# Kernel tuning notes

Hardware: AMD Instinct MI355X
Metric: run time of the kernel (lower is better)

Reference implementation:

```python
import jax, jax.numpy as jnp
import numpy as np

N_NODES = 100000
N_EDGES = 3200000
N_GRAPHS = 64
IN_DIM = 128
EDGE_DIM = 16
HIDDEN = 64
LATENT = 16


def setup_inputs() -> dict:
    key = jax.random.key(0)
    ks = jax.random.split(key, 12)
    x = jax.random.normal(ks[0], (N_NODES, IN_DIM), dtype=jnp.float32)
    edge_feat = jax.random.normal(ks[1], (N_EDGES, EDGE_DIM), dtype=jnp.float32)
    src = jax.random.randint(ks[2], (N_EDGES,), 0, N_NODES)
    dst = jax.random.randint(ks[3], (N_EDGES,), 0, N_NODES)
    node_graph = jnp.sort(jax.random.randint(ks[4], (N_NODES,), 0, N_GRAPHS))
    s = lambda d: 1.0 / np.sqrt(d)
    W1 = jax.random.normal(ks[5], (IN_DIM, HIDDEN), dtype=jnp.float32) * s(IN_DIM)
    b1 = jnp.zeros((HIDDEN,), jnp.float32)
    W2 = jax.random.normal(ks[6], (HIDDEN, HIDDEN), dtype=jnp.float32) * s(HIDDEN)
    b2 = jnp.zeros((HIDDEN,), jnp.float32)
    We = jax.random.normal(ks[7], (EDGE_DIM, HIDDEN), dtype=jnp.float32) * s(EDGE_DIM)
    be = jnp.zeros((HIDDEN,), jnp.float32)
    Wmu = jax.random.normal(ks[8], (HIDDEN, LATENT), dtype=jnp.float32) * s(HIDDEN)
    bmu = jnp.zeros((LATENT,), jnp.float32)
    Wlv = jax.random.normal(ks[9], (HIDDEN, LATENT), dtype=jnp.float32) * s(HIDDEN)
    blv = jnp.zeros((LATENT,), jnp.float32)
    return {"x": x, "edge_feat": edge_feat, "src": src, "dst": dst,
            "node_graph": node_graph, "W1": W1, "b1": b1, "W2": W2, "b2": b2,
            "We": We, "be": be, "Wmu": Wmu, "bmu": bmu, "Wlv": Wlv, "blv": blv}


def _graph_conv(h, src, dst, W, b):
    # DGL GraphConv with norm='both', allow_zero_in_degree=True, ReLU activation.
    ones = jnp.ones((src.shape[0],), h.dtype)
    deg_out = jnp.clip(jax.ops.segment_sum(ones, src, num_segments=N_NODES), 1.0)
    deg_in = jnp.clip(jax.ops.segment_sum(ones, dst, num_segments=N_NODES), 1.0)
    # project first (cheaper when out <= in), then symmetric-normalized SpMM
    hw = h @ W  # [N, out]
    hw = hw * (deg_out ** -0.5)[:, None]
    agg = jax.ops.segment_sum(hw[src], dst, num_segments=N_NODES)
    agg = agg * (deg_in ** -0.5)[:, None]
    return jax.nn.relu(agg + b)


def reference(x, edge_feat, src, dst, node_graph, W1, b1, W2, b2, We, be,
              Wmu, bmu, Wlv, blv):
    h = _graph_conv(x, src, dst, W1, b1)
    h = _graph_conv(h, src, dst, W2, b2)
    # edge_fc is computed and stored in edata in the original, but does not
    # affect the (mu, logvar) outputs
    edge_h = edge_feat @ We + be  # noqa: F841 (kept for fidelity)
    # dgl.mean_nodes: per-graph mean of node features
    sums = jax.ops.segment_sum(h, node_graph, num_segments=N_GRAPHS)
    counts = jnp.clip(jax.ops.segment_sum(jnp.ones((N_NODES,), h.dtype),
                                          node_graph, num_segments=N_GRAPHS), 1.0)
    h_graph = sums / counts[:, None]  # [G, HIDDEN]
    mu = h_graph @ Wmu + bmu
    logvar = h_graph @ Wlv + blv
    return (mu, logvar)
```

## Files before the change

kernel.cpp:

```cpp
#include <hip/hip_runtime.h>
#include <hip/hip_fp16.h>

#define N_NODES 100000
#define N_EDGES 3200000
#define N_GRAPHS 64
#define IN_DIM 128
#define HIDDEN 64
#define LATENT 16

#define NB 1024
#define BSH 7
#define NB_USED 782
#define SC_BLOCKS 256
#define NKEYS 1024
#define NBLK_AGG 1563
#define SEG_INTS (1565 * 64)

__global__ __launch_bounds__(256) void zero_k(int4* __restrict__ p, int n4) {
  int i = blockIdx.x * 256 + threadIdx.x;
  if (i < n4) p[i] = make_int4(0, 0, 0, 0);
}

__global__ __launch_bounds__(256) void hist_c_k(const int4* __restrict__ src4,
                                                const int4* __restrict__ dst4,
                                                int* __restrict__ bc_src,
                                                int* __restrict__ bc_dst,
                                                int* __restrict__ tbl_src,
                                                int* __restrict__ tbl_dst) {
  __shared__ int hs[NB], hd[NB];
  int t = threadIdx.x;
  for (int i = t; i < NB; i += 256) { hs[i] = 0; hd[i] = 0; }
  __syncthreads();
  const int Q = N_EDGES / 4;
  const int QPB = Q / SC_BLOCKS;
  int q0 = blockIdx.x * QPB, q1 = q0 + QPB;
  for (int i = q0 + t; i < q1; i += 256) {
    int4 s = src4[i], d = dst4[i];
    atomicAdd(&hs[s.x >> BSH], 1); atomicAdd(&hs[s.y >> BSH], 1);
    atomicAdd(&hs[s.z >> BSH], 1); atomicAdd(&hs[s.w >> BSH], 1);
    atomicAdd(&hd[d.x >> BSH], 1); atomicAdd(&hd[d.y >> BSH], 1);
    atomicAdd(&hd[d.z >> BSH], 1); atomicAdd(&hd[d.w >> BSH], 1);
  }
  __syncthreads();
  for (int i = t; i < NB; i += 256) {
    int a = hs[i], b = hd[i];
    tbl_src[blockIdx.x * NB + i] = a;
    tbl_dst[blockIdx.x * NB + i] = b;
    if (a) atomicAdd(&bc_src[i], a);
    if (b) atomicAdd(&bc_dst[i], b);
  }
}

__global__ __launch_bounds__(256) void scan_c_k(const int* __restrict__ bc_src,
                                                const int* __restrict__ bc_dst,
                                                int* __restrict__ bbase_src,
                                                int* __restrict__ bbase_dst) {
  __shared__ int ts[256];
  int t = threadIdx.x;
  int b4 = 4 * t;
  {
    int a0 = bc_src[b4], a1 = bc_src[b4 + 1], a2 = bc_src[b4 + 2], a3 = bc_src[b4 + 3];
    int s = a0 + a1 + a2 + a3;
    ts[t] = s;
    __syncthreads();
    for (int off = 1; off < 256; off <<= 1) {
      int x = 0;
      if (t >= off) x = ts[t - off];
      __syncthreads();
      if (t >= off) ts[t] += x;
      __syncthreads();
    }
    int run = ts[t] - s;
    bbase_src[b4] = run;
    bbase_src[b4 + 1] = run + a0;
    bbase_src[b4 + 2] = run + a0 + a1;
    bbase_src[b4 + 3] = run + a0 + a1 + a2;
    if (t == 255) bbase_src[NB] = ts[255];
    __syncthreads();
  }
  {
    int a0 = bc_dst[b4], a1 = bc_dst[b4 + 1], a2 = bc_dst[b4 + 2], a3 = bc_dst[b4 + 3];
    int s = a0 + a1 + a2 + a3;
    ts[t] = s;
    __syncthreads();
    for (int off = 1; off < 256; off <<= 1) {
      int x = 0;
      if (t >= off) x = ts[t - off];
      __syncthreads();
      if (t >= off) ts[t] += x;
      __syncthreads();
    }
    int run = ts[t] - s;
    bbase_dst[b4] = run;
    bbase_dst[b4 + 1] = run + a0;
    bbase_dst[b4 + 2] = run + a0 + a1;
    bbase_dst[b4 + 3] = run + a0 + a1 + a2;
    if (t == 255) bbase_dst[NB] = ts[255];
  }
}

__global__ __launch_bounds__(256) void scatter_c_k(const int4* __restrict__ src4,
                                                   const int4* __restrict__ dst4,
                                                   const int* __restrict__ bbase_src,
                                                   const int* __restrict__ bbase_dst,
                                                   const int* __restrict__ tbl_src,
                                                   const int* __restrict__ tbl_dst,
                                                   int* __restrict__ cur_src,
                                                   int* __restrict__ cur_dst,
                                                   int* __restrict__ sortedS,
                                                   int* __restrict__ sortedE) {
  __shared__ int rs[NB], rd[NB];
  int t = threadIdx.x;
  for (int i = t; i < NB; i += 256) {
    int a = tbl_src[blockIdx.x * NB + i];
    int b = tbl_dst[blockIdx.x * NB + i];
    rs[i] = a ? (atomicAdd(&cur_src[i], a) + bbase_src[i]) : 0;
    rd[i] = b ? (atomicAdd(&cur_dst[i], b) + bbase_dst[i]) : 0;
  }
  __syncthreads();
  const int Q = N_EDGES / 4;
  const int QPB = Q / SC_BLOCKS;
  int q0 = blockIdx.x * QPB, q1 = q0 + QPB;
  for (int i = q0 + t; i < q1; i += 256) {
    int4 s = src4[i], d = dst4[i];
    int sv[4] = {s.x, s.y, s.z, s.w};
    int dv[4] = {d.x, d.y, d.z, d.w};
#pragma unroll
    for (int k = 0; k < 4; k++) {
      int ps = atomicAdd(&rs[sv[k] >> BSH], 1);
      sortedS[ps] = sv[k];
      int pd = atomicAdd(&rd[dv[k] >> BSH], 1);
      sortedE[pd] = ((dv[k] & 127) << 17) | sv[k];
    }
  }
}

__global__ __launch_bounds__(256) void fine_sort_k(const int* __restrict__ sortedE,
                                                   const int* __restrict__ bbase_dst,
                                                   int* __restrict__ deg_in,
                                                   int* __restrict__ seg,
                                                   int* __restrict__ eblk) {
  __shared__ int hist[NKEYS];
  __shared__ int cur[NKEYS];
  __shared__ int ts[256];
  int bk = blockIdx.x, t = threadIdx.x;
  int node0 = bk << BSH;
  int e0 = bbase_dst[bk], e1 = bbase_dst[bk + 1];
  for (int i = t; i < NKEYS; i += 256) hist[i] = 0;
  __syncthreads();
  for (int j = e0 + t; j < e1; j += 256) {
    int v = sortedE[j];
    int d7 = v >> 17, sr = v & 0x1FFFF;
    int key = ((d7 >> 6) << 9) | ((sr >> 14) << 6) | ((d7 & 7) << 3) | ((d7 >> 3) & 7);
    atomicAdd(&hist[key], 1);
  }
  __syncthreads();
  int b4 = 4 * t;
  int a0 = hist[b4], a1 = hist[b4 + 1], a2 = hist[b4 + 2], a3 = hist[b4 + 3];
  int s = a0 + a1 + a2 + a3;
  ts[t] = s;
  __syncthreads();
  for (int off = 1; off < 256; off <<= 1) {
    int x = 0;
    if (t >= off) x = ts[t - off];
    __syncthreads();
    if (t >= off) ts[t] += x;
    __syncthreads();
  }
  int run = ts[t] - s;
  cur[b4] = run;
  cur[b4 + 1] = run + a0;
  cur[b4 + 2] = run + a0 + a1;
  cur[b4 + 3] = run + a0 + a1 + a2;
  __syncthreads();
  if (t < 128) {
    int n = node0 + t;
    if (n < N_NODES) {
      int sub = t >> 6, o = t & 7, row = (t >> 3) & 7;
      int base = (sub << 9) | (o << 3) | row;
      int dg = 0;
#pragma unroll
      for (int c = 0; c < 8; c++) dg += hist[base + (c << 6)];
      deg_in[n] = dg;
    }
  }
  if (t < 128) {
    int sub = t >> 6, c = (t >> 3) & 7, o = t & 7;
    seg[(bk * 2 + sub) * 64 + c * 8 + o] = e0 + cur[(sub << 9) | (c << 6) | (o << 3)];
  }
  __syncthreads();
  for (int j = e0 + t; j < e1; j += 256) {
    int v = sortedE[j];
    int d7 = v >> 17, sr = v & 0x1FFFF;
    int key = ((d7 >> 6) << 9) | ((sr >> 14) << 6) | ((d7 & 7) << 3) | ((d7 >> 3) & 7);
    int pos = e0 + atomicAdd(&cur[key], 1);
    eblk[pos] = ((d7 & 63) << 17) | sr;
  }
}

__global__ __launch_bounds__(256) void degout_c_k(const int* __restrict__ sortedS,
                                                  const int* __restrict__ bbase_src,
                                                  int* __restrict__ deg_out) {
  __shared__ int h[128];
  int bk = blockIdx.x, t = threadIdx.x;
  if (t < 128) h[t] = 0;
  __syncthreads();
  int s0 = bbase_src[bk], s1 = bbase_src[bk + 1];
  for (int j = s0 + t; j < s1; j += 256) atomicAdd(&h[sortedS[j] & 127], 1);
  __syncthreads();
  if (t < 128) {
    int n = (bk << BSH) | t;
    if (n < N_NODES) deg_out[n] = h[t];
  }
}

__global__ __launch_bounds__(256) void counts_k(const int* __restrict__ node_graph,
                                                float* __restrict__ counts) {
  __shared__ int h[N_GRAPHS];
  int t = threadIdx.x;
  if (t < N_GRAPHS) h[t] = 0;
  __syncthreads();
  int base = blockIdx.x * 1024;
  int end = base + 1024; if (end > N_NODES) end = N_NODES;
  for (int i = base + t; i < end; i += 256) atomicAdd(&h[node_graph[i]], 1);
  __syncthreads();
  if (t < N_GRAPHS && h[t]) atomicAdd(&counts[t], (float)h[t]);
}

template <int IN, typename IT, typename OT>
__global__ __launch_bounds__(256) void gemm_tile_k(const IT* __restrict__ X,
                                                   const float* __restrict__ W,
                                                   const int* __restrict__ deg,
                                                   OT* __restrict__ out) {
  __shared__ float xs[64][IN + 4];
  __shared__ float ws[IN][HIDDEN];
  int t = threadIdx.x;
  int row0_blk = blockIdx.x * 64;

  for (int i = t; i < IN * HIDDEN / 4; i += 256)
    ((float4*)ws)[i] = ((const float4*)W)[i];
  for (int i = t; i < 64 * (IN / 4); i += 256) {
    int r = i / (IN / 4), c4 = i % (IN / 4);
    int row = row0_blk + r;
    float4 v = make_float4(0.f, 0.f, 0.f, 0.f);
    if (row < N_NODES) {
      if constexpr (sizeof(IT) == 4) {
        v = *(const float4*)&X[(size_t)row * IN + c4 * 4];
      } else {
        union { short4 s; __half2 h2[2]; } u;
        u.s = *(const short4*)&X[(size_t)row * IN + c4 * 4];
        float2 f0 = __half22float2(u.h2[0]);
        float2 f1 = __half22float2(u.h2[1]);
        v = make_float4(f0.x, f0.y, f1.x, f1.y);
      }
    }
    *(float4*)&xs[r][c4 * 4] = v;
  }
  __syncthreads();

  int w = t >> 6, lane = t & 63;
  int rg = lane >> 4, cg = lane & 15;
  int r0 = w * 16 + rg * 4;
  int c0 = cg * 4;

  float acc[4][4];
#pragma unroll
  for (int i = 0; i < 4; i++)
#pragma unroll
    for (int j = 0; j < 4; j++) acc[i][j] = 0.f;

#pragma unroll 4
  for (int d4 = 0; d4 < IN / 4; d4++) {
    float4 a0 = *(const float4*)&xs[r0 + 0][d4 * 4];
    float4 a1 = *(const float4*)&xs[r0 + 1][d4 * 4];
    float4 a2 = *(const float4*)&xs[r0 + 2][d4 * 4];
    float4 a3 = *(const float4*)&xs[r0 + 3][d4 * 4];
#pragma unroll
    for (int dd = 0; dd < 4; dd++) {
      float4 b = *(const float4*)&ws[d4 * 4 + dd][c0];
      float av0 = (&a0.x)[dd], av1 = (&a1.x)[dd], av2 = (&a2.x)[dd], av3 = (&a3.x)[dd];
      acc[0][0] += av0 * b.x; acc[0][1] += av0 * b.y; acc[0][2] += av0 * b.z; acc[0][3] += av0 * b.w;
      acc[1][0] += av1 * b.x; acc[1][1] += av1 * b.y; acc[1][2] += av1 * b.z; acc[1][3] += av1 * b.w;
      acc[2][0] += av2 * b.x; acc[2][1] += av2 * b.y; acc[2][2] += av2 * b.z; acc[2][3] += av2 * b.w;
      acc[3][0] += av3 * b.x; acc[3][1] += av3 * b.y; acc[3][2] += av3 * b.z; acc[3][3] += av3 * b.w;
    }
  }

#pragma unroll
  for (int i = 0; i < 4; i++) {
    int row = row0_blk + r0 + i;
    if (row >= N_NODES) continue;
    float dg = (float)deg[row];
    if (dg < 1.f) dg = 1.f;
    float sc = rsqrtf(dg);
    if constexpr (sizeof(OT) == 2) {
      __half2 p0 = __floats2half2_rn(acc[i][0] * sc, acc[i][1] * sc);
      __half2 p1 = __floats2half2_rn(acc[i][2] * sc, acc[i][3] * sc);
      union { __half2 h2[2]; float2 f2; } u;
      u.h2[0] = p0; u.h2[1] = p1;
      *(float2*)&out[(size_t)row * HIDDEN + c0] = u.f2;
    } else {
      float4 o = make_float4(acc[i][0] * sc, acc[i][1] * sc, acc[i][2] * sc, acc[i][3] * sc);
      *(float4*)&out[(size_t)row * HIDDEN + c0] = o;
    }
  }
}

template <int MODE>
__global__ __launch_bounds__(256) void agg_seg_k(const __half* __restrict__ A,
                                                 const int* __restrict__ eblk,
                                                 const int* __restrict__ seg,
                                                 const int* __restrict__ deg_in,
                                                 const float* __restrict__ bias,
                                                 const float* __restrict__ W2,
                                                 const int* __restrict__ deg_out,
                                                 const int* __restrict__ node_graph,
                                                 float* __restrict__ sums,
                                                 __half* __restrict__ out) {
  __shared__ float acc[64][68];
  __shared__ int ngs[64];
  __shared__ float psum[4][64];
  int bk = blockIdx.x, t = threadIdx.x;
  int o = t >> 5, l = t & 31;
  for (int i = t; i < 64 * 68; i += 256) ((float*)acc)[i] = 0.f;
  __syncthreads();
  int segbase = bk * 64;
  float rx = 0.f, ry = 0.f;
  int cur_d = -1;
#pragma unroll
  for (int c = 0; c < 8; c++) {
    int j0 = seg[segbase + c * 8 + o];
    int j1 = seg[segbase + c * 8 + o + 1];
    int j = j0;
    for (; j + 16 <= j1; j += 16) {
      int ev = eblk[j + (l & 15)];
      int vv[16];
#pragma unroll
      for (int k = 0; k < 16; k++) vv[k] = __shfl(ev, k, 32);
      float2 ff[16];
#pragma unroll
      for (int k = 0; k < 16; k++)
        ff[k] = __half22float2(*(const __half2*)&A[(size_t)(vv[k] & 0x1FFFF) * HIDDEN + 2 * l]);
#pragma unroll
      for (int k = 0; k < 16; k++) {
        int d = vv[k] >> 17;
        if (d != cur_d) {
          if (cur_d >= 0) {
            float2* ap = (float2*)&acc[cur_d][2 * l];
            float2 a0 = *ap; a0.x += rx; a0.y += ry; *ap = a0;
          }
          cur_d = d; rx = 0.f; ry = 0.f;
        }
        rx += ff[k].x; ry += ff[k].y;
      }
    }
    for (; j + 4 <= j1; j += 4) {
      int vv[4];
#pragma unroll
      for (int k = 0; k < 4; k++) vv[k] = eblk[j + k];
      float2 ff[4];
#pragma unroll
      for (int k = 0; k < 4; k++)
        ff[k] = __half22float2(*(const __half2*)&A[(size_t)(vv[k] & 0x1FFFF) * HIDDEN + 2 * l]);
#pragma unroll
      for (int k = 0; k < 4; k++) {
        int d = vv[k] >> 17;
        if (d != cur_d) {
          if (cur_d >= 0) {
            float2* ap = (float2*)&acc[cur_d][2 * l];
            float2 a0 = *ap; a0.x += rx; a0.y += ry; *ap = a0;
          }
          cur_d = d; rx = 0.f; ry = 0.f;
        }
        rx += ff[k].x; ry += ff[k].y;
      }
    }
    for (; j < j1; j++) {
      int v = eblk[j];
      int d = v >> 17;
      if (d != cur_d) {
        if (cur_d >= 0) {
          float2* ap = (float2*)&acc[cur_d][2 * l];
          float2 a0 = *ap; a0.x += rx; a0.y += ry; *ap = a0;
        }
        cur_d = d; rx = 0.f; ry = 0.f;
      }
      float2 f = __half22float2(*(const __half2*)&A[(size_t)(v & 0x1FFFF) * HIDDEN + 2 * l]);
      rx += f.x; ry += f.y;
    }
  }
  if (cur_d >= 0) {
    float2* ap = (float2*)&acc[cur_d][2 * l];
    float2 a0 = *ap; a0.x += rx; a0.y += ry; *ap = a0;
  }
  __syncthreads();

  int node0 = bk << 6;
  if constexpr (MODE == 1) {
    for (int i = t; i < 64 * 64; i += 256) {
      int r = i >> 6, ch = i & 63;
      float dg = (float)deg_in[node0 + r];
      if (dg < 1.f) dg = 1.f;
      float v = acc[r][ch] * rsqrtf(dg) + bias[ch];
      acc[r][ch] = v > 0.f ? v : 0.f;
    }
    __syncthreads();
    int w = t >> 6, lane = t & 63;
    int rg = lane >> 4, cg = lane & 15;
    int r0 = w * 16 + rg * 4;
    int c0 = cg * 4;
    float oacc[4][4];
#pragma unroll
    for (int i = 0; i < 4; i++)
#pragma unroll
      for (int j = 0; j < 4; j++) oacc[i][j] = 0.f;
#pragma unroll 4
    for (int d = 0; d < 64; d++) {
      float4 b = *(const float4*)&W2[d * HIDDEN + c0];
      float a0 = acc[r0 + 0][d], a1 = acc[r0 + 1][d];
      float a2 = acc[r0 + 2][d], a3 = acc[r0 + 3][d];
      oacc[0][0] += a0 * b.x; oacc[0][1] += a0 * b.y; oacc[0][2] += a0 * b.z; oacc[0][3] += a0 * b.w;
      oacc[1][0] += a1 * b.x; oacc[1][1] += a1 * b.y; oacc[1][2] += a1 * b.z; oacc[1][3] += a1 * b.w;
      oacc[2][0] += a2 * b.x; oacc[2][1] += a2 * b.y; oacc[2][2] += a2 * b.z; oacc[2][3] += a2 * b.w;
      oacc[3][0] += a3 * b.x; oacc[3][1] += a3 * b.y; oacc[3][2] += a3 * b.z; oacc[3][3] += a3 * b.w;
    }
#pragma unroll
    for (int i = 0; i < 4; i++) {
      int node = node0 + r0 + i;
      if (node >= N_NODES) continue;
      float dg = (float)deg_out[node];
      if (dg < 1.f) dg = 1.f;
      float sc = rsqrtf(dg);
      __half2 p0 = __floats2half2_rn(oacc[i][0] * sc, oacc[i][1] * sc);
      __half2 p1 = __floats2half2_rn(oacc[i][2] * sc, oacc[i][3] * sc);
      union { __half2 h2[2]; float2 f2; } u;
      u.h2[0] = p0; u.h2[1] = p1;
      *(float2*)&out[(size_t)node * HIDDEN + c0] = u.f2;
    }
  } else {
    if (t < 64) {
      int node = node0 + t;
      ngs[t] = (node < N_NODES) ? node_graph[node] : -1;
    }
    __syncthreads();
    int ch = t & 63, q = t >> 6;
    bool uniform = (ngs[0] >= 0) && (ngs[0] == ngs[63]);
    if (uniform) {
      float a = 0.f;
      for (int r = q * 16; r < q * 16 + 16; r++) {
        float dg = (float)deg_in[node0 + r];
        if (dg < 1.f) dg = 1.f;
        float v = acc[r][ch] * rsqrtf(dg) + bias[ch];
        a += (v > 0.f ? v : 0.f);
      }
      psum[q][ch] = a;
      __syncthreads();
      if (t < 64) {
        float s4 = psum[0][t] + psum[1][t] + psum[2][t] + psum[3][t];
        atomicAdd(&sums[ngs[0] * HIDDEN + t], s4);
      }
    } else {
      int curg = -1; float a = 0.f;
      for (int r = q * 16; r < q * 16 + 16; r++) {
        int g = ngs[r];
        if (g != curg) {
          if (curg >= 0) atomicAdd(&sums[curg * HIDDEN + ch], a);
          curg = g; a = 0.f;
        }
        if (g >= 0) {
          float dg = (float)deg_in[node0 + r];
          if (dg < 1.f) dg = 1.f;
          float v = acc[r][ch] * rsqrtf(dg) + bias[ch];
          a += (v > 0.f ? v : 0.f);
        }
      }
      if (curg >= 0) atomicAdd(&sums[curg * HIDDEN + ch], a);
    }
  }
}

__global__ __launch_bounds__(256) void final_k(const float* __restrict__ sums,
                                               const float* __restrict__ counts,
                                               const float* __restrict__ Wmu,
                                               const float* __restrict__ bmu,
                                               const float* __restrict__ Wlv,
                                               const float* __restrict__ blv,
                                               float* __restrict__ out) {
  __shared__ float hg[N_GRAPHS][HIDDEN];
  __shared__ float wmu[HIDDEN][LATENT];
  __shared__ float wlv[HIDDEN][LATENT];
  int t = threadIdx.x;
  for (int i = t; i < N_GRAPHS * HIDDEN; i += 256) {
    int g = i / HIDDEN;
    float c = counts[g];
    if (c < 1.f) c = 1.f;
    hg[g][i % HIDDEN] = sums[i] / c;
  }
  for (int i = t; i < HIDDEN * LATENT; i += 256) {
    wmu[i / LATENT][i % LATENT] = Wmu[i];
    wlv[i / LATENT][i % LATENT] = Wlv[i];
  }
  __syncthreads();
  for (int i = t; i < N_GRAPHS * LATENT; i += 256) {
    int g = i / LATENT, j = i % LATENT;
    float mu = bmu[j], lv = blv[j];
#pragma unroll
    for (int k = 0; k < HIDDEN; k++) {
      float v = hg[g][k];
      mu += v * wmu[k][j];
      lv += v * wlv[k][j];
    }
    out[i] = mu;
    out[N_GRAPHS * LATENT + i] = lv;
  }
}

extern "C" void kernel_launch(void* const* d_in, const int* in_sizes, int n_in,
                              void* d_out, int out_size, void* d_ws, size_t ws_size,
                              hipStream_t stream) {
  const float* x = (const float*)d_in[0];
  const int* src = (const int*)d_in[2];
  const int* dst = (const int*)d_in[3];
  const int* node_graph = (const int*)d_in[4];
  const float* W1 = (const float*)d_in[5];
  const float* b1 = (const float*)d_in[6];
  const float* W2 = (const float*)d_in[7];
  const float* b2 = (const float*)d_in[8];
  const float* Wmu = (const float*)d_in[11];
  const float* bmu = (const float*)d_in[12];
  const float* Wlv = (const float*)d_in[13];
  const float* blv = (const float*)d_in[14];
  float* out = (float*)d_out;

  char* ws = (char*)d_ws;
  int* bc_src   = (int*)(ws + 0);
  int* bc_dst   = (int*)(ws + 4096);
  int* cur_src  = (int*)(ws + 8192);
  int* cur_dst  = (int*)(ws + 12288);
  float* cnts   = (float*)(ws + 16384);
  float* sums   = (float*)(ws + 16896);
  int* bbase_src = (int*)(ws + 33280);
  int* bbase_dst = (int*)(ws + 37632);
  int* tbl_src   = (int*)(ws + 41984);
  int* tbl_dst   = (int*)(ws + 1090560);
  int* deg_out = (int*)(ws + 2139136);
  int* deg_in  = (int*)(ws + 2539264);
  int* seg     = (int*)(ws + 2939392);
  int* eblk    = (int*)(ws + 3340800);
  int* sortedS = (int*)(ws + 16140800);
  int* sortedE = (int*)(ws + 28940800);
  __half* A1   = (__half*)(ws + 16140800);
  __half* A2   = (__half*)(ws + 28940800);

  zero_k<<<(33280 / 16 + 255) / 256, 256, 0, stream>>>((int4*)ws, 33280 / 16);

  hist_c_k<<<SC_BLOCKS, 256, 0, stream>>>((const int4*)src, (const int4*)dst,
                                          bc_src, bc_dst, tbl_src, tbl_dst);
  scan_c_k<<<1, 256, 0, stream>>>(bc_src, bc_dst, bbase_src, bbase_dst);
  scatter_c_k<<<SC_BLOCKS, 256, 0, stream>>>((const int4*)src, (const int4*)dst,
                                             bbase_src, bbase_dst, tbl_src, tbl_dst,
                                             cur_src, cur_dst, sortedS, sortedE);
  fine_sort_k<<<NB_USED, 256, 0, stream>>>(sortedE, bbase_dst, deg_in, seg, eblk);
  degout_c_k<<<NB_USED, 256, 0, stream>>>(sortedS, bbase_src, deg_out);
  counts_k<<<(N_NODES + 1023) / 1024, 256, 0, stream>>>(node_graph, cnts);

  const int GEMM_BLKS = (N_NODES + 63) / 64;

  gemm_tile_k<IN_DIM, float, __half><<<GEMM_BLKS, 256, 0, stream>>>(x, W1, deg_out, A1);
  agg_seg_k<1><<<NBLK_AGG, 256, 0, stream>>>(A1, eblk, seg, deg_in, b1, W2, deg_out,
                                             nullptr, nullptr, A2);
  agg_seg_k<2><<<NBLK_AGG, 256, 0, stream>>>(A2, eblk, seg, deg_in, b2, nullptr, nullptr,
                                             node_graph, sums, nullptr);

  final_k<<<1, 256, 0, stream>>>(sums, cnts, Wmu, bmu, Wlv, blv, out);
}
```

Before: 363.4 us.

## Fuse graph counts into degout, read X directly in GEMM, prefetch edge indices

Merges the per-graph node count histogram into the out-degree kernel, which removes one kernel launch. The first GEMM no longer stages X tiles in shared memory; each thread loads its four rows straight from global memory, freeing LDS and dropping a barrier at the cost of less coalesced, redundant loads. The aggregation loop now prefetches the next 16 edge indices while the current batch is processed, to hide index-load latency.

```diff
diff --git a/kernel.cpp b/kernel.cpp
--- a/kernel.cpp
+++ b/kernel.cpp
@@ -200,68 +200,47 @@
 
 __global__ __launch_bounds__(256) void degout_c_k(const int* __restrict__ sortedS,
                                                   const int* __restrict__ bbase_src,
-                                                  int* __restrict__ deg_out) {
+                                                  const int* __restrict__ node_graph,
+                                                  int* __restrict__ deg_out,
+                                                  float* __restrict__ counts) {
   __shared__ int h[128];
+  __shared__ int hg[N_GRAPHS];
   int bk = blockIdx.x, t = threadIdx.x;
   if (t < 128) h[t] = 0;
+  if (t < N_GRAPHS) hg[t] = 0;
   __syncthreads();
   int s0 = bbase_src[bk], s1 = bbase_src[bk + 1];
   for (int j = s0 + t; j < s1; j += 256) atomicAdd(&h[sortedS[j] & 127], 1);
+  if (t < 128) {
+    int n = (bk << BSH) | t;
+    if (n < N_NODES) atomicAdd(&hg[node_graph[n]], 1);
+  }
   __syncthreads();
   if (t < 128) {
     int n = (bk << BSH) | t;
     if (n < N_NODES) deg_out[n] = h[t];
   }
-}
-
-__global__ __launch_bounds__(256) void counts_k(const int* __restrict__ node_graph,
-                                                float* __restrict__ counts) {
-  __shared__ int h[N_GRAPHS];
-  int t = threadIdx.x;
-  if (t < N_GRAPHS) h[t] = 0;
-  __syncthreads();
-  int base = blockIdx.x * 1024;
-  int end = base + 1024; if (end > N_NODES) end = N_NODES;
-  for (int i = base + t; i < end; i += 256) atomicAdd(&h[node_graph[i]], 1);
-  __syncthreads();
-  if (t < N_GRAPHS && h[t]) atomicAdd(&counts[t], (float)h[t]);
-}
-
-template <int IN, typename IT, typename OT>
-__global__ __launch_bounds__(256) void gemm_tile_k(const IT* __restrict__ X,
-                                                   const float* __restrict__ W,
-                                                   const int* __restrict__ deg,
-                                                   OT* __restrict__ out) {
-  __shared__ float xs[64][IN + 4];
-  __shared__ float ws[IN][HIDDEN];
+  if (t < N_GRAPHS && hg[t]) atomicAdd(&counts[t], (float)hg[t]);
+}
+
+__global__ __launch_bounds__(256) void gemm1_k(const float* __restrict__ X,
+                                               const float* __restrict__ W,
+                                               const int* __restrict__ deg,
+                                               __half* __restrict__ out) {
+  __shared__ float ws[IN_DIM][HIDDEN];
   int t = threadIdx.x;
   int row0_blk = blockIdx.x * 64;
 
-  for (int i = t; i < IN * HIDDEN / 4; i += 256)
+  for (int i = t; i < IN_DIM * HIDDEN / 4; i += 256)
     ((float4*)ws)[i] = ((const float4*)W)[i];
-  for (int i = t; i < 64 * (IN / 4); i += 256) {
-    int r = i / (IN / 4), c4 = i % (IN / 4);
-    int row = row0_blk + r;
-    float4 v = make_float4(0.f, 0.f, 0.f, 0.f);
-    if (row < N_NODES) {
-      if constexpr (sizeof(IT) == 4) {
-        v = *(const float4*)&X[(size_t)row * IN + c4 * 4];
-      } else {
-        union { short4 s; __half2 h2[2]; } u;
-        u.s = *(const short4*)&X[(size_t)row * IN + c4 * 4];
-        float2 f0 = __half22float2(u.h2[0]);
-        float2 f1 = __half22float2(u.h2[1]);
-        v = make_float4(f0.x, f0.y, f1.x, f1.y);
-      }
-    }
-    *(float4*)&xs[r][c4 * 4] = v;
-  }
   __syncthreads();
 
   int w = t >> 6, lane = t & 63;
   int rg = lane >> 4, cg = lane & 15;
   int r0 = w * 16 + rg * 4;
   int c0 = cg * 4;
+  int row_base = row0_blk + r0;
+  bool full = (row_base + 3 < N_NODES);
 
   float acc[4][4];
 #pragma unroll
@@ -269,12 +248,21 @@
 #pragma unroll
     for (int j = 0; j < 4; j++) acc[i][j] = 0.f;
 
+  const float zero4[4] = {0.f, 0.f, 0.f, 0.f};
 #pragma unroll 4
-  for (int d4 = 0; d4 < IN / 4; d4++) {
-    float4 a0 = *(const float4*)&xs[r0 + 0][d4 * 4];
-    float4 a1 = *(const float4*)&xs[r0 + 1][d4 * 4];
-    float4 a2 = *(const float4*)&xs[r0 + 2][d4 * 4];
-    float4 a3 = *(const float4*)&xs[r0 + 3][d4 * 4];
+  for (int d4 = 0; d4 < IN_DIM / 4; d4++) {
+    float4 a0, a1, a2, a3;
+    if (full) {
+      a0 = *(const float4*)&X[(size_t)(row_base + 0) * IN_DIM + d4 * 4];
+      a1 = *(const float4*)&X[(size_t)(row_base + 1) * IN_DIM + d4 * 4];
+      a2 = *(const float4*)&X[(size_t)(row_base + 2) * IN_DIM + d4 * 4];
+      a3 = *(const float4*)&X[(size_t)(row_base + 3) * IN_DIM + d4 * 4];
+    } else {
+      a0 = (row_base + 0 < N_NODES) ? *(const float4*)&X[(size_t)(row_base + 0) * IN_DIM + d4 * 4] : *(const float4*)zero4;
+      a1 = (row_base + 1 < N_NODES) ? *(const float4*)&X[(size_t)(row_base + 1) * IN_DIM + d4 * 4] : *(const float4*)zero4;
+      a2 = (row_base + 2 < N_NODES) ? *(const float4*)&X[(size_t)(row_base + 2) * IN_DIM + d4 * 4] : *(const float4*)zero4;
+      a3 = (row_base + 3 < N_NODES) ? *(const float4*)&X[(size_t)(row_base + 3) * IN_DIM + d4 * 4] : *(const float4*)zero4;
+    }
 #pragma unroll
     for (int dd = 0; dd < 4; dd++) {
       float4 b = *(const float4*)&ws[d4 * 4 + dd][c0];
@@ -288,21 +276,16 @@
 
 #pragma unroll
   for (int i = 0; i < 4; i++) {
-    int row = row0_blk + r0 + i;
+    int row = row_base + i;
     if (row >= N_NODES) continue;
     float dg = (float)deg[row];
     if (dg < 1.f) dg = 1.f;
     float sc = rsqrtf(dg);
-    if constexpr (sizeof(OT) == 2) {
-      __half2 p0 = __floats2half2_rn(acc[i][0] * sc, acc[i][1] * sc);
-      __half2 p1 = __floats2half2_rn(acc[i][2] * sc, acc[i][3] * sc);
-      union { __half2 h2[2]; float2 f2; } u;
-      u.h2[0] = p0; u.h2[1] = p1;
-      *(float2*)&out[(size_t)row * HIDDEN + c0] = u.f2;
-    } else {
-      float4 o = make_float4(acc[i][0] * sc, acc[i][1] * sc, acc[i][2] * sc, acc[i][3] * sc);
-      *(float4*)&out[(size_t)row * HIDDEN + c0] = o;
-    }
+    __half2 p0 = __floats2half2_rn(acc[i][0] * sc, acc[i][1] * sc);
+    __half2 p1 = __floats2half2_rn(acc[i][2] * sc, acc[i][3] * sc);
+    union { __half2 h2[2]; float2 f2; } u;
+    u.h2[0] = p0; u.h2[1] = p1;
+    *(float2*)&out[(size_t)row * HIDDEN + c0] = u.f2;
   }
 }
 
@@ -332,11 +315,14 @@
     int j0 = seg[segbase + c * 8 + o];
     int j1 = seg[segbase + c * 8 + o + 1];
     int j = j0;
-    for (; j + 16 <= j1; j += 16) {
-      int ev = eblk[j + (l & 15)];
+    int ev = (j + 16 <= j1) ? eblk[j + (l & 15)] : 0;
+    for (; j + 16 <= j1; ) {
+      int ev_cur = ev;
+      int jn = j + 16;
+      if (jn + 16 <= j1) ev = eblk[jn + (l & 15)];
       int vv[16];
 #pragma unroll
-      for (int k = 0; k < 16; k++) vv[k] = __shfl(ev, k, 32);
+      for (int k = 0; k < 16; k++) vv[k] = __shfl(ev_cur, k, 32);
       float2 ff[16];
 #pragma unroll
       for (int k = 0; k < 16; k++)
@@ -353,6 +339,7 @@
         }
         rx += ff[k].x; ry += ff[k].y;
       }
+      j = jn;
     }
     for (; j + 4 <= j1; j += 4) {
       int vv[4];
@@ -561,12 +548,11 @@
                                              bbase_src, bbase_dst, tbl_src, tbl_dst,
                                              cur_src, cur_dst, sortedS, sortedE);
   fine_sort_k<<<NB_USED, 256, 0, stream>>>(sortedE, bbase_dst, deg_in, seg, eblk);
-  degout_c_k<<<NB_USED, 256, 0, stream>>>(sortedS, bbase_src, deg_out);
-  counts_k<<<(N_NODES + 1023) / 1024, 256, 0, stream>>>(node_graph, cnts);
+  degout_c_k<<<NB_USED, 256, 0, stream>>>(sortedS, bbase_src, node_graph, deg_out, cnts);
 
   const int GEMM_BLKS = (N_NODES + 63) / 64;
 
-  gemm_tile_k<IN_DIM, float, __half><<<GEMM_BLKS, 256, 0, stream>>>(x, W1, deg_out, A1);
+  gemm1_k<<<GEMM_BLKS, 256, 0, stream>>>(x, W1, deg_out, A1);
   agg_seg_k<1><<<NBLK_AGG, 256, 0, stream>>>(A1, eblk, seg, deg_in, b1, W2, deg_out,
                                              nullptr, nullptr, A2);
   agg_seg_k<2><<<NBLK_AGG, 256, 0, stream>>>(A2, eblk, seg, deg_in, b2, nullptr, nullptr,
```

Measured after the change: 312.7 us (median of 2 runs). 13.9% less time.
